# Performance work log

Hardware: AMD Instinct MI355X
Metric: run time of the kernel (lower is better)

The kernel has to match this reference:

```python
import jax, jax.numpy as jnp
import numpy as np

NUM_CLASSES = 1000
TEMPERATURE = 0.1
B, B_OOD, D = 4096, 4096, 512


def _l2norm(x):
    return x / jnp.linalg.norm(x, axis=-1, keepdims=True)


def setup_inputs() -> dict:
    key = jax.random.key(0)
    k1, k2, k3, k4, k5 = jax.random.split(key, 5)
    return {
        "centers1": _l2norm(jax.random.normal(k1, (NUM_CLASSES, D), dtype=jnp.float32)),
        "features": _l2norm(jax.random.normal(k2, (B, D), dtype=jnp.float32)),
        "targets": jax.random.randint(k3, (B,), 0, NUM_CLASSES, dtype=jnp.int64 if jax.config.jax_enable_x64 else jnp.int32),
        "features_ood": _l2norm(jax.random.normal(k4, (B_OOD, D), dtype=jnp.float32)),
        "pseudo_target_ood": jax.random.randint(k5, (B_OOD,), 0, NUM_CLASSES, dtype=jnp.int64 if jax.config.jax_enable_x64 else jnp.int32),
    }


def reference(centers1, features, targets, features_ood, pseudo_target_ood):
    C = centers1.shape[0]
    b = features.shape[0]
    bo = features_ood.shape[0]
    n = b + C + bo  # total anchors: batch + class centers + ood

    centers_lbl = jnp.arange(C, dtype=targets.dtype)
    ood_lbl = jnp.full((bo,), C, dtype=targets.dtype)  # ood gets label == num_classes
    targets_all = jnp.concatenate([targets, centers_lbl, ood_lbl])              # [N]
    targets_all_class = jnp.concatenate([targets, centers_lbl, pseudo_target_ood])  # [N]

    # per-class count over all N labels (pseudo labels for ood)
    batch_cls_count = jnp.zeros((C,), dtype=jnp.float32).at[targets_all_class].add(1.0)

    # positive mask: same label as anchor, excluding self (diagonal for j < B)
    mask = (targets_all[:b, None] == targets_all[None, :]).astype(jnp.float32)  # [B,N]
    logits_mask = 1.0 - (jnp.arange(n)[None, :] == jnp.arange(b)[:, None]).astype(jnp.float32)
    mask = mask * logits_mask

    features_all = jnp.concatenate([features, centers1, features_ood], axis=0)  # [N,D]
    logits = jnp.matmul(features, features_all.T) / TEMPERATURE                 # [B,N]
    logits = logits - jax.lax.stop_gradient(jnp.max(logits, axis=1, keepdims=True))

    exp_logits = jnp.exp(logits) * logits_mask
    # class-balanced per-instance weight (count of the column's class, minus positive mask)
    per_ins_weight = batch_cls_count[targets_all_class][None, :] - mask         # [B,N]
    exp_logits_sum = jnp.sum(exp_logits / per_ins_weight, axis=1, keepdims=True)
    log_prob = logits - jnp.log(exp_logits_sum)

    mean_log_prob_pos = jnp.sum(mask * log_prob, axis=1) / jnp.sum(mask, axis=1)
    loss = -jnp.mean(mean_log_prob_pos)
    return loss
```

## Files before the change

kernel.cpp:

```cpp
#include <hip/hip_runtime.h>
#include <stdint.h>

#define NUM_C 1000
#define NB    4096
#define NCOL  9192
#define NPAD  9216
#define DK    512
#define BM    128
#define BN    256
#define INV_T 10.0f

typedef __attribute__((ext_vector_type(16))) float f32x16;
typedef __attribute__((ext_vector_type(8)))  int   i32x8;

#define OFF_FALL  0u
#define OFF_CNT   4718592u
#define OFF_CNTT  4722688u
#define OFF_S     4726784u
#define OFF_P     4743168u

#define NCHUNKBLK 1152

__device__ __forceinline__ void async16(const void* g, void* l) {
  __builtin_amdgcn_global_load_lds((const __attribute__((address_space(1))) void*)g,
                                   (__attribute__((address_space(3))) void*)l,
                                   16, 0, 0);
}

__device__ __forceinline__ unsigned sw_e4m3(float x) {
  float ax = fabsf(x);
  unsigned s = (__float_as_uint(x) >> 24) & 0x80u;
  if (ax < 0.015625f) {
    int n = (int)rintf(ax * 512.0f);
    if (n >= 8) return s | 0x08u;
    return s | (unsigned)n;
  }
  if (ax >= 448.0f) return s | 0x7Eu;
  unsigned u = __float_as_uint(ax);
  int ee = (int)(u >> 23) - 127;
  float scale = __uint_as_float((unsigned)(3 - ee + 127) << 23);
  int qv = (int)rintf(ax * scale);
  if (qv == 16) { ee++; qv = 8; }
  return s | (unsigned)(((ee + 7) << 3) | (qv - 8));
}

template <bool HI>
__device__ __forceinline__ int cvt2(float a, float b, int old) {
#if __has_builtin(__builtin_amdgcn_cvt_pk_fp8_f32)
  return __builtin_amdgcn_cvt_pk_fp8_f32(a, b, old, HI);
#else
  unsigned pk = sw_e4m3(a) | (sw_e4m3(b) << 8);
  return HI ? (int)(((unsigned)old & 0x0000FFFFu) | (pk << 16))
            : (int)(((unsigned)old & 0xFFFF0000u) | pk);
#endif
}

__device__ __forceinline__ i32x8 mk8(uint4 lo, uint4 hi) {
  i32x8 r;
  r[0] = (int)lo.x; r[1] = (int)lo.y; r[2] = (int)lo.z; r[3] = (int)lo.w;
  r[4] = (int)hi.x; r[5] = (int)hi.y; r[6] = (int)hi.z; r[7] = (int)hi.w;
  return r;
}

#define MFMA_SC(a, b, c) \
  __builtin_amdgcn_mfma_scale_f32_32x32x64_f8f6f4((a), (b), (c), 0, 0, 0, 0x7F7F7F7F, 0, 0x7F7F7F7F)

__global__ __launch_bounds__(256) void prep_k(const float* __restrict__ centers,
                                              const float* __restrict__ feats,
                                              const float* __restrict__ ood,
                                              const int* __restrict__ targets,
                                              const int* __restrict__ pseudo,
                                              uint4* __restrict__ fall,
                                              unsigned* __restrict__ cnt,
                                              unsigned* __restrict__ cntT,
                                              float* __restrict__ SP) {
  __shared__ unsigned hc[1024];
  __shared__ unsigned hct[1024];
  const int tid = threadIdx.x;

  if (blockIdx.x < NCHUNKBLK) {
    int idx  = blockIdx.x * 256 + tid;
    int tile = idx >> 10;
    int kq   = (idx >> 7) & 7;
    int p    = idx & 127;
    int c    = p ^ ((p >> 3) & 7);
    int lane = c >> 1;
    int row  = tile * 32 + (lane & 31);
    int k0   = kq * 64 + (lane >> 5) * 32 + (c & 1) * 16;

    const float* src = nullptr;
    if (row < NB)              src = feats   + (size_t)row * DK;
    else if (row < NB + NUM_C) src = centers + (size_t)(row - NB) * DK;
    else if (row < NCOL)       src = ood     + (size_t)(row - NB - NUM_C) * DK;
    uint4 out = make_uint4(0u, 0u, 0u, 0u);
    if (src) {
      float4 v0 = *(const float4*)(src + k0);
      float4 v1 = *(const float4*)(src + k0 + 4);
      float4 v2 = *(const float4*)(src + k0 + 8);
      float4 v3 = *(const float4*)(src + k0 + 12);
      int q;
      q = 0; q = cvt2<false>(v0.x, v0.y, q); q = cvt2<true>(v0.z, v0.w, q); out.x = (unsigned)q;
      q = 0; q = cvt2<false>(v1.x, v1.y, q); q = cvt2<true>(v1.z, v1.w, q); out.y = (unsigned)q;
      q = 0; q = cvt2<false>(v2.x, v2.y, q); q = cvt2<true>(v2.z, v2.w, q); out.z = (unsigned)q;
      q = 0; q = cvt2<false>(v3.x, v3.y, q); q = cvt2<true>(v3.z, v3.w, q); out.w = (unsigned)q;
    }
    fall[idx] = out;

    if (blockIdx.x < 32)
      SP[blockIdx.x * 256 + tid] = 0.0f;
  } else {
    for (int kk = tid; kk < 1024; kk += 256) { hc[kk] = 0u; hct[kk] = 0u; }
    __syncthreads();
    for (int i = tid; i < NB; i += 256) {
      int tt = targets[i];
      atomicAdd(&hc[tt], 1u);
      atomicAdd(&hct[tt], 1u);
      atomicAdd(&hc[pseudo[i]], 1u);
    }
    __syncthreads();
    for (int kk = tid; kk < 1024; kk += 256) {
      cnt[kk]  = hc[kk];
      cntT[kk] = hct[kk];
    }
  }
}

__global__ __launch_bounds__(256, 2) void gemm_fused(const unsigned char* __restrict__ fall,
                                                     const int* __restrict__ targets,
                                                     const int* __restrict__ pseudo,
                                                     const unsigned* __restrict__ cnt,
                                                     float* __restrict__ Sacc,
                                                     float* __restrict__ Pacc) {
  __shared__ unsigned char Alds[65536];
  __shared__ int    sLbl[BN];
  __shared__ float  sRw0[BN];
  __shared__ float  sRw1[BN];
  __shared__ int    sTgt[BM];

  const int tid  = threadIdx.x;
  int flat = (int)blockIdx.y * 36 + (int)blockIdx.x;
  int swz  = (flat & 7) * 144 + (flat >> 3);
  const int nTile = swz >> 5;
  const int mTile = swz & 31;
  const int lane  = tid & 63;
  const int wv    = tid >> 6;

  {
    const unsigned char* aSrc = fall + (size_t)mTile * 65536;
#pragma unroll
    for (int i = 0; i < 16; i++)
      async16(aSrc + (i * 256 + tid) * 16, &Alds[(i * 256 + tid) * 16]);
  }

  {
    int j = nTile * BN + tid;
    int lbl, tac;
    if (j >= NCOL)         { lbl = -1; tac = -1; }
    else if (j < NB)       { tac = targets[j]; lbl = tac; }
    else if (j < NB+NUM_C) { tac = j - NB;     lbl = tac; }
    else                   { tac = pseudo[j - NB - NUM_C]; lbl = NUM_C; }
    sLbl[tid] = lbl;
    if (tac >= 0) {
      float w = (float)(1u + cnt[tac]);
      sRw0[tid] = 1.0f / w;
      sRw1[tid] = 1.0f / (w - 1.0f);
    } else {
      sRw0[tid] = 0.f;
      sRw1[tid] = 0.f;
    }
    if (tid < BM) sTgt[tid] = targets[mTile * BM + tid];
  }

  f32x16 acc[4][2];
  {
    f32x16 z;
#pragma unroll
    for (int t = 0; t < 16; t++) z[t] = 0.f;
#pragma unroll
    for (int mi = 0; mi < 4; mi++) { acc[mi][0] = z; acc[mi][1] = z; }
  }

  const int swzo = ((lane >> 2) & 7) << 4;
  const int off0 = (lane << 5) ^ swzo;
  const int off1 = off0 ^ 16;

  const unsigned char* bBase0 = fall + (size_t)(nTile * 8 + wv * 2) * 16384;
  const unsigned char* bBase1 = bBase0 + 16384;

  uint4 bb[2][4];
#pragma unroll
  for (int s = 0; s < 2; s++) {
    const unsigned char* pb0 = bBase0 + s * 2048;
    const unsigned char* pb1 = bBase1 + s * 2048;
    bb[s][0] = *(const uint4*)(pb0 + off0);
    bb[s][1] = *(const uint4*)(pb0 + off1);
    bb[s][2] = *(const uint4*)(pb1 + off0);
    bb[s][3] = *(const uint4*)(pb1 + off1);
  }

  __syncthreads();

#pragma unroll
  for (int kq = 0; kq < 8; kq++) {
    const int sl = kq & 1;
    i32x8 bf0 = mk8(bb[sl][0], bb[sl][1]);
    i32x8 bf1 = mk8(bb[sl][2], bb[sl][3]);
    if (kq < 6) {
      const unsigned char* pb0 = bBase0 + (kq + 2) * 2048;
      const unsigned char* pb1 = bBase1 + (kq + 2) * 2048;
      bb[sl][0] = *(const uint4*)(pb0 + off0);
      bb[sl][1] = *(const uint4*)(pb0 + off1);
      bb[sl][2] = *(const uint4*)(pb1 + off0);
      bb[sl][3] = *(const uint4*)(pb1 + off1);
    }
#pragma unroll
    for (int mi = 0; mi < 4; mi++) {
      const unsigned ao = (unsigned)mi * 16384u + (unsigned)kq * 2048u;
      uint4 al = *(const uint4*)&Alds[ao + off0];
      uint4 ah = *(const uint4*)&Alds[ao + off1];
      i32x8 af = mk8(al, ah);
      acc[mi][0] = MFMA_SC(af, bf0, acc[mi][0]);
      acc[mi][1] = MFMA_SC(af, bf1, acc[mi][1]);
    }
  }

  const int cq = lane & 31;
  const int hh = lane >> 5;
  const int jl0 = wv * 64 + cq;
  const int jl1 = jl0 + 32;
  const int jg0 = nTile * BN + jl0;
  const int jg1 = jg0 + 32;
  const int lbl0 = sLbl[jl0], lbl1 = sLbl[jl1];
  const float w00 = sRw0[jl0], w01 = sRw1[jl0];
  const float w10 = sRw0[jl1], w11 = sRw1[jl1];

  float* sS = (float*)Alds;
  float* sP = (float*)(Alds + 512);
  __syncthreads();
  if (tid < BM) { sS[tid] = 0.f; sP[tid] = 0.f; }
  __syncthreads();

#define RED(m, s, h)                                           \
  {                                                            \
    float sSv = (lane & (m)) ? vS[(s)] : vS[(s) + (h)];        \
    float sPv = (lane & (m)) ? vP[(s)] : vP[(s) + (h)];        \
    float rS = __shfl_xor(sSv, (m), 64);                       \
    float rP = __shfl_xor(sPv, (m), 64);                       \
    vS[(s)] = ((lane & (m)) ? vS[(s) + (h)] : vS[(s)]) + rS;   \
    vP[(s)] = ((lane & (m)) ? vP[(s) + (h)] : vP[(s)]) + rP;   \
  }

#pragma unroll
  for (int mi = 0; mi < 4; mi++) {
    float vS[16], vP[16];
#pragma unroll
    for (int r = 0; r < 16; r++) {
      int rowT = (r & 3) + 8 * (r >> 2) + 4 * hh;
      int iloc = mi * 32 + rowT;
      int ig   = mTile * BM + iloc;
      int ti   = sTgt[iloc];
      float l0 = acc[mi][0][r] * INV_T;
      float l1 = acc[mi][1][r] * INV_T;
      bool d0 = (jg0 == ig), d1 = (jg1 == ig);
      bool p0 = (lbl0 == ti) && !d0;
      bool p1 = (lbl1 == ti) && !d1;
      float r0 = d0 ? 0.f : (p0 ? w01 : w00);
      float r1 = d1 ? 0.f : (p1 ? w11 : w10);
      vS[r] = __expf(l0 - 10.0f) * r0 + __expf(l1 - 10.0f) * r1;
      vP[r] = (p0 ? l0 : 0.f) + (p1 ? l1 : 0.f);
    }
    RED(1, 0, 8) RED(1, 1, 8) RED(1, 2, 8) RED(1, 3, 8)
    RED(1, 4, 8) RED(1, 5, 8) RED(1, 6, 8) RED(1, 7, 8)
    RED(2, 0, 4) RED(2, 1, 4) RED(2, 2, 4) RED(2, 3, 4)
    RED(4, 0, 2) RED(4, 1, 2)
    RED(8, 0, 1)
    {
      int rr   = ((lane & 1) << 3) | ((lane & 2) << 1) | ((lane & 4) >> 1) | ((lane & 8) >> 3);
      int rowT = (rr & 3) + 8 * (rr >> 2) + 4 * hh;
      int iloc = mi * 32 + rowT;
      atomicAdd(&sS[iloc], vS[0]);
      atomicAdd(&sP[iloc], vP[0]);
    }
  }
#undef RED

  __syncthreads();
  if (tid < BM) {
    int ig = mTile * BM + tid;
    atomicAdd(&Sacc[ig], sS[tid]);
    atomicAdd(&Pacc[ig], sP[tid]);
  }
}

__global__ __launch_bounds__(256) void finalize_k(const float* __restrict__ S,
                                                  const float* __restrict__ P,
                                                  const int* __restrict__ targets,
                                                  const unsigned* __restrict__ cntT,
                                                  float* __restrict__ out) {
  __shared__ unsigned ct[1024];
  __shared__ float red[4];
  int tid = threadIdx.x;
  for (int k = tid; k < 1024; k += 256) ct[k] = cntT[k];
  __syncthreads();
  float local = 0.f;
  for (int i = tid; i < NB; i += 256) {
    float npos = (float)ct[targets[i]];
    local += P[i] / npos - INV_T - __logf(S[i]);
  }
  for (int m = 1; m < 64; m <<= 1) local += __shfl_xor(local, m, 64);
  if ((tid & 63) == 0) red[tid >> 6] = local;
  __syncthreads();
  if (tid == 0) {
    float t = red[0] + red[1] + red[2] + red[3];
    out[0] = -t / (float)NB;
  }
}

extern "C" void kernel_launch(void* const* d_in, const int* in_sizes, int n_in,
                              void* d_out, int out_size, void* d_ws, size_t ws_size,
                              hipStream_t stream) {
  const float* centers = (const float*)d_in[0];
  const float* feats   = (const float*)d_in[1];
  const int*   targets = (const int*)d_in[2];
  const float* ood     = (const float*)d_in[3];
  const int*   pseudo  = (const int*)d_in[4];

  char* ws = (char*)d_ws;
  uint4*    fall  = (uint4*)(ws + OFF_FALL);
  unsigned* cnt   = (unsigned*)(ws + OFF_CNT);
  unsigned* cntT  = (unsigned*)(ws + OFF_CNTT);
  float*    Sacc  = (float*)(ws + OFF_S);
  float*    Pacc  = (float*)(ws + OFF_P);

  prep_k<<<dim3(NCHUNKBLK + 1), 256, 0, stream>>>(centers, feats, ood, targets, pseudo,
                                                  fall, cnt, cntT, Sacc);
  gemm_fused<<<dim3(NPAD / BN, NB / BM), 256, 0, stream>>>((const unsigned char*)fall, targets,
                                                           pseudo, cnt, Sacc, Pacc);
  finalize_k<<<1, 256, 0, stream>>>(Sacc, Pacc, targets, cntT, (float*)d_out);
}
```

Before: 132.1 us.

## Use 8 waves per GEMM block with swapped MFMA operands and shuffle-free epilogue

The fused GEMM block grows from 4 to 8 waves, arranged 2x4 over M and N, so each wave owns a 64x64 sub-tile instead of 128x64. MFMA operands are swapped so each lane's accumulator column corresponds to one row, which lets the epilogue sum per lane directly instead of running the cross-lane shuffle reduction tree. Column metadata is packed into a single int4 table, and the histogram block in prep_k moves to block 0 so it is scheduled first. In exchange, twice as many waves re-read the same B data from global memory and contend for LDS, and register pressure under the 512-thread launch bound may limit occupancy.

```diff
diff --git a/kernel.cpp b/kernel.cpp
--- a/kernel.cpp
+++ b/kernel.cpp
@@ -78,8 +78,8 @@
   __shared__ unsigned hct[1024];
   const int tid = threadIdx.x;
 
-  if (blockIdx.x < NCHUNKBLK) {
-    int idx  = blockIdx.x * 256 + tid;
+  if (blockIdx.x > 0) {
+    int idx  = (blockIdx.x - 1) * 256 + tid;
     int tile = idx >> 10;
     int kq   = (idx >> 7) & 7;
     int p    = idx & 127;
@@ -106,8 +106,8 @@
     }
     fall[idx] = out;
 
-    if (blockIdx.x < 32)
-      SP[blockIdx.x * 256 + tid] = 0.0f;
+    if (blockIdx.x <= 32)
+      SP[(blockIdx.x - 1) * 256 + tid] = 0.0f;
   } else {
     for (int kk = tid; kk < 1024; kk += 256) { hc[kk] = 0u; hct[kk] = 0u; }
     __syncthreads();
@@ -125,17 +125,17 @@
   }
 }
 
-__global__ __launch_bounds__(256, 2) void gemm_fused(const unsigned char* __restrict__ fall,
+__global__ __launch_bounds__(512, 4) void gemm_fused(const unsigned char* __restrict__ fall,
                                                      const int* __restrict__ targets,
                                                      const int* __restrict__ pseudo,
                                                      const unsigned* __restrict__ cnt,
                                                      float* __restrict__ Sacc,
                                                      float* __restrict__ Pacc) {
   __shared__ unsigned char Alds[65536];
-  __shared__ int    sLbl[BN];
-  __shared__ float  sRw0[BN];
-  __shared__ float  sRw1[BN];
+  __shared__ int4   sTab[BN];
   __shared__ int    sTgt[BM];
+  __shared__ float  sS[BM];
+  __shared__ float  sP[BM];
 
   const int tid  = threadIdx.x;
   int flat = (int)blockIdx.y * 36 + (int)blockIdx.x;
@@ -144,47 +144,50 @@
   const int mTile = swz & 31;
   const int lane  = tid & 63;
   const int wv    = tid >> 6;
+  const int wm    = wv >> 2;
+  const int wn    = wv & 3;
 
   {
     const unsigned char* aSrc = fall + (size_t)mTile * 65536;
 #pragma unroll
-    for (int i = 0; i < 16; i++)
-      async16(aSrc + (i * 256 + tid) * 16, &Alds[(i * 256 + tid) * 16]);
-  }
-
-  {
+    for (int i = 0; i < 8; i++)
+      async16(aSrc + (i * 512 + tid) * 16, &Alds[(i * 512 + tid) * 16]);
+  }
+
+  if (tid < BN) {
     int j = nTile * BN + tid;
     int lbl, tac;
     if (j >= NCOL)         { lbl = -1; tac = -1; }
     else if (j < NB)       { tac = targets[j]; lbl = tac; }
     else if (j < NB+NUM_C) { tac = j - NB;     lbl = tac; }
     else                   { tac = pseudo[j - NB - NUM_C]; lbl = NUM_C; }
-    sLbl[tid] = lbl;
+    float r0 = 0.f, r1 = 0.f;
     if (tac >= 0) {
       float w = (float)(1u + cnt[tac]);
-      sRw0[tid] = 1.0f / w;
-      sRw1[tid] = 1.0f / (w - 1.0f);
-    } else {
-      sRw0[tid] = 0.f;
-      sRw1[tid] = 0.f;
-    }
-    if (tid < BM) sTgt[tid] = targets[mTile * BM + tid];
-  }
-
-  f32x16 acc[4][2];
+      r0 = 1.0f / w;
+      r1 = 1.0f / (w - 1.0f);
+    }
+    sTab[tid] = make_int4(lbl, __float_as_int(r0), __float_as_int(r1), 0);
+  } else if (tid < BN + BM) {
+    int i = tid - BN;
+    sTgt[i] = targets[mTile * BM + i];
+    sS[i] = 0.f;
+    sP[i] = 0.f;
+  }
+
+  f32x16 acc00, acc01, acc10, acc11;
   {
     f32x16 z;
 #pragma unroll
     for (int t = 0; t < 16; t++) z[t] = 0.f;
-#pragma unroll
-    for (int mi = 0; mi < 4; mi++) { acc[mi][0] = z; acc[mi][1] = z; }
+    acc00 = z; acc01 = z; acc10 = z; acc11 = z;
   }
 
   const int swzo = ((lane >> 2) & 7) << 4;
   const int off0 = (lane << 5) ^ swzo;
   const int off1 = off0 ^ 16;
 
-  const unsigned char* bBase0 = fall + (size_t)(nTile * 8 + wv * 2) * 16384;
+  const unsigned char* bBase0 = fall + (size_t)(nTile * 8 + wn * 2) * 16384;
   const unsigned char* bBase1 = bBase0 + 16384;
 
   uint4 bb[2][4];
@@ -213,76 +216,67 @@
       bb[sl][2] = *(const uint4*)(pb1 + off0);
       bb[sl][3] = *(const uint4*)(pb1 + off1);
     }
-#pragma unroll
-    for (int mi = 0; mi < 4; mi++) {
-      const unsigned ao = (unsigned)mi * 16384u + (unsigned)kq * 2048u;
+    {
+      const unsigned ao = (unsigned)(wm * 2 + 0) * 16384u + (unsigned)kq * 2048u;
       uint4 al = *(const uint4*)&Alds[ao + off0];
       uint4 ah = *(const uint4*)&Alds[ao + off1];
       i32x8 af = mk8(al, ah);
-      acc[mi][0] = MFMA_SC(af, bf0, acc[mi][0]);
-      acc[mi][1] = MFMA_SC(af, bf1, acc[mi][1]);
+      acc00 = MFMA_SC(bf0, af, acc00);
+      acc01 = MFMA_SC(bf1, af, acc01);
+    }
+    {
+      const unsigned ao = (unsigned)(wm * 2 + 1) * 16384u + (unsigned)kq * 2048u;
+      uint4 al = *(const uint4*)&Alds[ao + off0];
+      uint4 ah = *(const uint4*)&Alds[ao + off1];
+      i32x8 af = mk8(al, ah);
+      acc10 = MFMA_SC(bf0, af, acc10);
+      acc11 = MFMA_SC(bf1, af, acc11);
     }
   }
 
   const int cq = lane & 31;
   const int hh = lane >> 5;
-  const int jl0 = wv * 64 + cq;
-  const int jl1 = jl0 + 32;
-  const int jg0 = nTile * BN + jl0;
-  const int jg1 = jg0 + 32;
-  const int lbl0 = sLbl[jl0], lbl1 = sLbl[jl1];
-  const float w00 = sRw0[jl0], w01 = sRw1[jl0];
-  const float w10 = sRw0[jl1], w11 = sRw1[jl1];
-
-  float* sS = (float*)Alds;
-  float* sP = (float*)(Alds + 512);
-  __syncthreads();
-  if (tid < BM) { sS[tid] = 0.f; sP[tid] = 0.f; }
-  __syncthreads();
-
-#define RED(m, s, h)                                           \
-  {                                                            \
-    float sSv = (lane & (m)) ? vS[(s)] : vS[(s) + (h)];        \
-    float sPv = (lane & (m)) ? vP[(s)] : vP[(s) + (h)];        \
-    float rS = __shfl_xor(sSv, (m), 64);                       \
-    float rP = __shfl_xor(sPv, (m), 64);                       \
-    vS[(s)] = ((lane & (m)) ? vS[(s) + (h)] : vS[(s)]) + rS;   \
-    vP[(s)] = ((lane & (m)) ? vP[(s) + (h)] : vP[(s)]) + rP;   \
-  }
-
-#pragma unroll
-  for (int mi = 0; mi < 4; mi++) {
-    float vS[16], vP[16];
+  const int iloc0 = wm * 64 + cq;
+  const int iloc1 = iloc0 + 32;
+  const int ig0 = mTile * BM + iloc0;
+  const int ig1 = mTile * BM + iloc1;
+  const int ti0 = sTgt[iloc0];
+  const int ti1 = sTgt[iloc1];
+
+  float s0 = 0.f, s1 = 0.f, p0 = 0.f, p1 = 0.f;
+#pragma unroll
+  for (int nj = 0; nj < 2; nj++) {
 #pragma unroll
     for (int r = 0; r < 16; r++) {
-      int rowT = (r & 3) + 8 * (r >> 2) + 4 * hh;
-      int iloc = mi * 32 + rowT;
-      int ig   = mTile * BM + iloc;
-      int ti   = sTgt[iloc];
-      float l0 = acc[mi][0][r] * INV_T;
-      float l1 = acc[mi][1][r] * INV_T;
-      bool d0 = (jg0 == ig), d1 = (jg1 == ig);
-      bool p0 = (lbl0 == ti) && !d0;
-      bool p1 = (lbl1 == ti) && !d1;
-      float r0 = d0 ? 0.f : (p0 ? w01 : w00);
-      float r1 = d1 ? 0.f : (p1 ? w11 : w10);
-      vS[r] = __expf(l0 - 10.0f) * r0 + __expf(l1 - 10.0f) * r1;
-      vP[r] = (p0 ? l0 : 0.f) + (p1 ? l1 : 0.f);
-    }
-    RED(1, 0, 8) RED(1, 1, 8) RED(1, 2, 8) RED(1, 3, 8)
-    RED(1, 4, 8) RED(1, 5, 8) RED(1, 6, 8) RED(1, 7, 8)
-    RED(2, 0, 4) RED(2, 1, 4) RED(2, 2, 4) RED(2, 3, 4)
-    RED(4, 0, 2) RED(4, 1, 2)
-    RED(8, 0, 1)
-    {
-      int rr   = ((lane & 1) << 3) | ((lane & 2) << 1) | ((lane & 4) >> 1) | ((lane & 8) >> 3);
-      int rowT = (rr & 3) + 8 * (rr >> 2) + 4 * hh;
-      int iloc = mi * 32 + rowT;
-      atomicAdd(&sS[iloc], vS[0]);
-      atomicAdd(&sP[iloc], vP[0]);
-    }
-  }
-#undef RED
+      int jl = wn * 64 + nj * 32 + (r & 3) + 8 * (r >> 2) + 4 * hh;
+      int jg = nTile * BN + jl;
+      int4 tb = sTab[jl];
+      float rw0 = __int_as_float(tb.y);
+      float rw1 = __int_as_float(tb.z);
+      float a0 = nj ? acc01[r] : acc00[r];
+      float a1 = nj ? acc11[r] : acc10[r];
+      {
+        bool d = (jg == ig0);
+        bool pp = (tb.x == ti0) && !d;
+        float rw = d ? 0.f : (pp ? rw1 : rw0);
+        float e = __expf(fmaf(a0, INV_T, -INV_T));
+        s0 = fmaf(e, rw, s0);
+        p0 += pp ? a0 : 0.f;
+      }
+      {
+        bool d = (jg == ig1);
+        bool pp = (tb.x == ti1) && !d;
+        float rw = d ? 0.f : (pp ? rw1 : rw0);
+        float e = __expf(fmaf(a1, INV_T, -INV_T));
+        s1 = fmaf(e, rw, s1);
+        p1 += pp ? a1 : 0.f;
+      }
+    }
+  }
+  atomicAdd(&sS[iloc0], s0);
+  atomicAdd(&sP[iloc0], p0 * INV_T);
+  atomicAdd(&sS[iloc1], s1);
+  atomicAdd(&sP[iloc1], p1 * INV_T);
 
   __syncthreads();
   if (tid < BM) {
@@ -334,7 +328,7 @@
 
   prep_k<<<dim3(NCHUNKBLK + 1), 256, 0, stream>>>(centers, feats, ood, targets, pseudo,
                                                   fall, cnt, cntT, Sacc);
-  gemm_fused<<<dim3(NPAD / BN, NB / BM), 256, 0, stream>>>((const unsigned char*)fall, targets,
+  gemm_fused<<<dim3(NPAD / BN, NB / BM), 512, 0, stream>>>((const unsigned char*)fall, targets,
                                                            pseudo, cnt, Sacc, Pacc);
   finalize_k<<<1, 256, 0, stream>>>(Sacc, Pacc, targets, cntT, (float*)d_out);
 }
```

Result: faster. 125.2 us (-5.2%).
